# Kernel tuning notes

Measured on AMD Instinct MI355X. Metric: run time of the kernel, lower is better.

The kernel has to match this reference:

```python
import jax, jax.numpy as jnp
import numpy as np

B, T, E = 2, 4096, 256
H = 4
HD = E // H
W = 65  # local_size, odd window


def setup_inputs() -> dict:
    key = jax.random.key(0)
    ks = jax.random.split(key, 5)
    s = 1.0 / np.sqrt(E)
    return {
        "x": jax.random.normal(ks[0], (B, T, E), dtype=jnp.float32),
        "Wqkv": jax.random.normal(ks[1], (3 * E, E), dtype=jnp.float32) * s,
        "bqkv": jax.random.normal(ks[2], (3 * E,), dtype=jnp.float32) * s,
        "Wout": jax.random.normal(ks[3], (E, E), dtype=jnp.float32) * s,
        "bout": jax.random.normal(ks[4], (E,), dtype=jnp.float32) * s,
    }


def _to_heads(t):
    # (B, T, E) -> (B*H, T, HD), head index = b*H + h (matches torch view/transpose)
    return t.reshape(B, T, H, HD).transpose(0, 2, 1, 3).reshape(B * H, T, HD)


def reference(x, Wqkv, bqkv, Wout, bout):
    scaling = float(HD) ** (-0.5)
    qkv = x @ Wqkv.T + bqkv                       # (B, T, 3E)
    q, k, v = jnp.split(qkv, 3, axis=-1)
    q = _to_heads(q * scaling)                    # (BH, T, HD)
    k = _to_heads(k)
    v = _to_heads(v)
    pad = (W - 1) // 2
    kp = jnp.pad(k, ((0, 0), (pad, pad), (0, 0)))  # (BH, T+W-1, HD)
    vp = jnp.pad(v, ((0, 0), (pad, pad), (0, 0)))
    idx = jnp.arange(T)[:, None] + jnp.arange(W)[None, :]  # (T, W)
    kw = kp[:, idx, :]                            # (BH, T, W, HD) overlapping windows
    vw = vp[:, idx, :]
    scores = jnp.einsum('btd,btwd->btw', q, kw)   # (BH, T, W)
    attn = jax.nn.softmax(scores, axis=-1)
    out = jnp.einsum('btw,btwd->btd', attn, vw)   # (BH, T, HD)
    out = out.reshape(B, H, T, HD).transpose(0, 2, 1, 3).reshape(B, T, E)
    return out @ Wout.T + bout
```

## Files before the change

### kernel.cpp

```cpp
#include <hip/hip_runtime.h>
#include <hip/hip_bf16.h>
#include <math.h>

#define T_   4096
#define E_   256
#define H_   4
#define HD_  64

typedef __attribute__((ext_vector_type(8))) short short8;
typedef __attribute__((ext_vector_type(4))) float f32x4;
typedef unsigned int u32;
typedef unsigned short ushort_t;

typedef const __attribute__((address_space(1))) u32* gas_ptr;
typedef __attribute__((address_space(3))) u32* las_ptr;

__device__ __forceinline__ void gld_lds16(const void* g, void* l) {
    __builtin_amdgcn_global_load_lds((gas_ptr)g, (las_ptr)l, 16, 0, 0);
}

__device__ __forceinline__ float bf_lo(u32 w) { return __uint_as_float(w << 16); }
__device__ __forceinline__ float bf_hi(u32 w) { return __uint_as_float(w & 0xffff0000u); }
__device__ __forceinline__ ushort_t f2bf(float f) {
    __hip_bfloat16 h = __float2bfloat16(f);
    return *reinterpret_cast<ushort_t*>(&h);
}

__global__ __launch_bounds__(256) void cvt_kernel(
    const float* __restrict__ x, const float* __restrict__ wq,
    const float* __restrict__ wo,
    ushort_t* __restrict__ xb, ushort_t* __restrict__ wqb, ushort_t* __restrict__ wob)
{
    int idx = blockIdx.x * 256 + threadIdx.x;
    const float* src; ushort_t* dst; int off;
    if (idx < 262144)       { src = x;  dst = xb;  off = idx * 8; }
    else if (idx < 286720)  { src = wq; dst = wqb; off = (idx - 262144) * 8; }
    else                    { src = wo; dst = wob; off = (idx - 286720) * 8; }
    float4 a = *(const float4*)(src + off);
    float4 b = *(const float4*)(src + off + 4);
    short8 p;
    p[0] = (short)f2bf(a.x); p[1] = (short)f2bf(a.y);
    p[2] = (short)f2bf(a.z); p[3] = (short)f2bf(a.w);
    p[4] = (short)f2bf(b.x); p[5] = (short)f2bf(b.y);
    p[6] = (short)f2bf(b.z); p[7] = (short)f2bf(b.w);
    *(short8*)(dst + off) = p;
}

template<int MODE>
__global__ __launch_bounds__(256) void gemm_kernel(
    const char* __restrict__ A, const char* __restrict__ Bw,
    const float* __restrict__ bias,
    ushort_t* __restrict__ o0, ushort_t* __restrict__ o1, ushort_t* __restrict__ o2,
    float* __restrict__ of)
{
    __shared__ __align__(16) char As[2][16384];
    __shared__ __align__(16) char Bs[2][8192];
    const int tid  = threadIdx.x;
    const int lane = tid & 63;
    const int wid  = tid >> 6;
    const int m0   = blockIdx.y * 128;
    const int bx   = blockIdx.x;
    const int n0   = bx * 64;

    f32x4 acc[2][4];
    #pragma unroll
    for (int i = 0; i < 2; ++i)
        #pragma unroll
        for (int j = 0; j < 4; ++j)
            acc[i][j] = (f32x4){0.f, 0.f, 0.f, 0.f};

    auto stage = [&](int buf, int ks) {
        const int kb = ks * 128;
        #pragma unroll
        for (int i = 0; i < 4; ++i) {
            int u   = wid * 4 + i;
            int o   = u * 1024 + lane * 16;
            int row = o >> 7;
            int cb  = o & 127;
            int sc  = cb ^ ((row & 7) << 4);
            gld_lds16(A + (size_t)(m0 + row) * 512 + kb + sc, &As[buf][u * 1024]);
        }
        #pragma unroll
        for (int i = 0; i < 2; ++i) {
            int u   = wid * 2 + i;
            int o   = u * 1024 + lane * 16;
            int row = o >> 7;
            int cb  = o & 127;
            int sc  = cb ^ ((row & 7) << 4);
            gld_lds16(Bw + (size_t)(n0 + row) * 512 + kb + sc, &Bs[buf][u * 1024]);
        }
    };

    auto compute = [&](int buf) {
        #pragma unroll
        for (int k2 = 0; k2 < 2; ++k2) {
            short8 af[2], bfr[4];
            #pragma unroll
            for (int mf = 0; mf < 2; ++mf) {
                int row = wid * 32 + mf * 16 + (lane & 15);
                int off = (k2 * 64 + (lane >> 4) * 16) ^ ((row & 7) << 4);
                af[mf] = *(const short8*)(&As[buf][row * 128 + off]);
            }
            #pragma unroll
            for (int nf = 0; nf < 4; ++nf) {
                int row = nf * 16 + (lane & 15);
                int off = (k2 * 64 + (lane >> 4) * 16) ^ ((row & 7) << 4);
                bfr[nf] = *(const short8*)(&Bs[buf][row * 128 + off]);
            }
            #pragma unroll
            for (int mf = 0; mf < 2; ++mf)
                #pragma unroll
                for (int nf = 0; nf < 4; ++nf)
                    acc[mf][nf] = __builtin_amdgcn_mfma_f32_16x16x32_bf16(
                        af[mf], bfr[nf], acc[mf][nf], 0, 0, 0);
        }
    };

    stage(0, 0);
    __syncthreads();
    #pragma unroll
    for (int t = 0; t < 4; ++t) {
        if (t < 3) stage((t + 1) & 1, t + 1);
        compute(t & 1);
        __syncthreads();
    }

    if (MODE == 0) {
        const int which = bx >> 2;
        const int h     = bx & 3;
        ushort_t* dst = (which == 0) ? o0 : (which == 1) ? o1 : o2;
        const float scale = (which == 0) ? 0.125f : 1.0f;
        #pragma unroll
        for (int nf = 0; nf < 4; ++nf) {
            int d = nf * 16 + (lane & 15);
            float bv = bias[n0 + d];
            #pragma unroll
            for (int mf = 0; mf < 2; ++mf)
                #pragma unroll
                for (int r = 0; r < 4; ++r) {
                    int m  = m0 + wid * 32 + mf * 16 + (lane >> 4) * 4 + r;
                    int bb = m >> 12;
                    int t  = m & (T_ - 1);
                    float v = (acc[mf][nf][r] + bv) * scale;
                    dst[((size_t)(bb * H_ + h) * T_ + t) * HD_ + d] = f2bf(v);
                }
        }
    } else {
        #pragma unroll
        for (int nf = 0; nf < 4; ++nf) {
            int n = n0 + nf * 16 + (lane & 15);
            float bv = bias[n];
            #pragma unroll
            for (int mf = 0; mf < 2; ++mf)
                #pragma unroll
                for (int r = 0; r < 4; ++r) {
                    int m = m0 + wid * 32 + mf * 16 + (lane >> 4) * 4 + r;
                    of[(size_t)m * E_ + n] = acc[mf][nf][r] + bv;
                }
        }
    }
}

__global__ __launch_bounds__(256) void attn_kernel(
    const ushort_t* __restrict__ q, const ushort_t* __restrict__ k,
    const ushort_t* __restrict__ v, ushort_t* __restrict__ ao)
{
    __shared__ __align__(16) char smem[20480 + 25600];
    char* Ks = smem;
    char* Pb = smem;
    char* Vt = smem + 20480;

    const int tid = threadIdx.x;
    const int bh  = blockIdx.y;
    const int t0  = blockIdx.x * 64;
    const int kbase = t0 - 32;
    const char* kb = (const char*)(k + (size_t)bh * T_ * HD_);
    const char* vb = (const char*)(v + (size_t)bh * T_ * HD_);
    const char* qb = (const char*)(q + (size_t)bh * T_ * HD_);

    int4 kreg[5], vreg[5];
    #pragma unroll
    for (int l = 0; l < 5; ++l) {
        int u = tid + l * 256;
        int row = u >> 3;
        int g = kbase + row;
        bool ok = (unsigned)g < (unsigned)T_;
        kreg[l] = ok ? *(const int4*)(kb + (size_t)g * 128 + (u & 7) * 16)
                     : make_int4(0, 0, 0, 0);
        vreg[l] = ok ? *(const int4*)(vb + (size_t)g * 128 + (u & 7) * 16)
                     : make_int4(0, 0, 0, 0);
    }
    #pragma unroll
    for (int l = 0; l < 5; ++l) {
        int u = tid + l * 256;
        int row = u >> 3;
        int cb = (u & 7) * 16;
        *(int4*)(Ks + row * 128 + (cb ^ ((row & 7) << 4))) = kreg[l];
        const u32* wv = (const u32*)&vreg[l];
        #pragma unroll
        for (int j = 0; j < 8; ++j) {
            int d = (u & 7) * 8 + j;
            ushort_t h = (j & 1) ? (ushort_t)(wv[j >> 1] >> 16)
                                 : (ushort_t)(wv[j >> 1] & 0xffffu);
            *(ushort_t*)(Vt + d * 400 + ((row * 2) ^ (((d >> 3) & 7) << 4))) = h;
        }
    }
    __syncthreads();

    const int wv_ = tid >> 6;
    const int ln  = tid & 15;
    const int lg  = (tid & 63) >> 4;

    short8 qf[2];
    #pragma unroll
    for (int k2 = 0; k2 < 2; ++k2)
        qf[k2] = *(const short8*)(qb + (size_t)(t0 + wv_ * 16 + ln) * 128
                                  + k2 * 64 + lg * 16);

    f32x4 sa[6];
    #pragma unroll
    for (int nf = 0; nf < 6; ++nf) sa[nf] = (f32x4){0.f, 0.f, 0.f, 0.f};
    #pragma unroll
    for (int k2 = 0; k2 < 2; ++k2) {
        #pragma unroll
        for (int nf = 0; nf < 6; ++nf) {
            int row = wv_ * 16 + nf * 16 + ln;
            short8 kf = *(const short8*)(Ks + row * 128 +
                          ((k2 * 64 + lg * 16) ^ ((row & 7) << 4)));
            sa[nf] = __builtin_amdgcn_mfma_f32_16x16x32_bf16(qf[k2], kf, sa[nf], 0, 0, 0);
        }
    }

    const int nm0 = ln - 4 * lg;
    #pragma unroll
    for (int nf = 0; nf < 6; ++nf)
        #pragma unroll
        for (int r = 0; r < 4; ++r) {
            int diff = nm0 + 16 * nf - r;
            if (diff < 0 || diff > 64) sa[nf][r] = -1e30f;
        }
    float inv_[4];
    #pragma unroll
    for (int r = 0; r < 4; ++r) {
        float mx = sa[0][r];
        #pragma unroll
        for (int nf = 1; nf < 6; ++nf) mx = fmaxf(mx, sa[nf][r]);
        mx = fmaxf(mx, __shfl_xor(mx, 1));
        mx = fmaxf(mx, __shfl_xor(mx, 2));
        mx = fmaxf(mx, __shfl_xor(mx, 4));
        mx = fmaxf(mx, __shfl_xor(mx, 8));
        float s = 0.f;
        #pragma unroll
        for (int nf = 0; nf < 6; ++nf) {
            float e = __expf(sa[nf][r] - mx);
            sa[nf][r] = e;
            s += e;
        }
        s += __shfl_xor(s, 1);
        s += __shfl_xor(s, 2);
        s += __shfl_xor(s, 4);
        s += __shfl_xor(s, 8);
        inv_[r] = 1.f / s;
    }

    __syncthreads();
    char* Pw = Pb + wv_ * 3328;
    #pragma unroll
    for (int nf = 0; nf < 6; ++nf)
        #pragma unroll
        for (int r = 0; r < 4; ++r)
            *(ushort_t*)(Pw + (4 * lg + r) * 208 + (16 * nf + ln) * 2)
                = f2bf(sa[nf][r]);

    f32x4 oa[4];
    #pragma unroll
    for (int nf = 0; nf < 4; ++nf) oa[nf] = (f32x4){0.f, 0.f, 0.f, 0.f};
    #pragma unroll
    for (int ks = 0; ks < 3; ++ks) {
        short8 pa = *(const short8*)(Pw + ln * 208 + ks * 64 + lg * 16);
        #pragma unroll
        for (int nf = 0; nf < 4; ++nf) {
            int d = nf * 16 + ln;
            short8 vbf = *(const short8*)(Vt + d * 400 +
                           ((32 * wv_ + 64 * ks + 16 * lg) ^ (((d >> 3) & 7) << 4)));
            oa[nf] = __builtin_amdgcn_mfma_f32_16x16x32_bf16(pa, vbf, oa[nf], 0, 0, 0);
        }
    }

    const int bb = bh >> 2, hh = bh & 3;
    #pragma unroll
    for (int nf = 0; nf < 4; ++nf)
        #pragma unroll
        for (int r = 0; r < 4; ++r) {
            int t = t0 + wv_ * 16 + 4 * lg + r;
            int d = nf * 16 + ln;
            ao[((size_t)bb * T_ + t) * E_ + hh * HD_ + d] = f2bf(oa[nf][r] * inv_[r]);
        }
}

extern "C" void kernel_launch(void* const* d_in, const int* in_sizes, int n_in,
                              void* d_out, int out_size, void* d_ws, size_t ws_size,
                              hipStream_t stream) {
    const float* x    = (const float*)d_in[0];
    const float* Wqkv = (const float*)d_in[1];
    const float* bqkv = (const float*)d_in[2];
    const float* Wout = (const float*)d_in[3];
    const float* bout = (const float*)d_in[4];
    float* out = (float*)d_out;

    char* ws = (char*)d_ws;
    ushort_t* xb  = (ushort_t*)(ws);
    ushort_t* wqb = (ushort_t*)(ws + 4194304);
    ushort_t* wob = (ushort_t*)(ws + 4587520);
    ushort_t* qb  = (ushort_t*)(ws + 4718592);
    ushort_t* kbp = (ushort_t*)(ws + 8912896);
    ushort_t* vbp = (ushort_t*)(ws + 13107200);
    ushort_t* aob = (ushort_t*)(ws + 17301504);

    cvt_kernel<<<1152, 256, 0, stream>>>(x, Wqkv, Wout, xb, wqb, wob);
    gemm_kernel<0><<<dim3(12, 64), 256, 0, stream>>>(
        (const char*)xb, (const char*)wqb, bqkv, qb, kbp, vbp, nullptr);
    attn_kernel<<<dim3(64, 8), 256, 0, stream>>>(qb, kbp, vbp, aob);
    gemm_kernel<1><<<dim3(4, 64), 256, 0, stream>>>(
        (const char*)aob, (const char*)wob, bout, nullptr, nullptr, nullptr, out);
}
```

Before: 34.46 us.

## Shrink GEMM M-tile to 64 and load full K slab at once

The GEMM kernel drops from 128-row tiles with a double-buffered K loop to 64-row tiles that load the whole K=256 slab of A and B into 64 KB of LDS in one shot, then run 8 MFMA steps. The grid doubles in the M dimension, so there are twice as many blocks to fill the CUs, and the per-step pipeline syncs go away. In exchange there is no overlap between loads and compute inside a block, B is reloaded twice as often, and the larger LDS footprint lowers occupancy per CU.

```diff
diff --git a/kernel.cpp b/kernel.cpp
--- a/kernel.cpp
+++ b/kernel.cpp
@@ -19,8 +19,6 @@
     __builtin_amdgcn_global_load_lds((gas_ptr)g, (las_ptr)l, 16, 0, 0);
 }
 
-__device__ __forceinline__ float bf_lo(u32 w) { return __uint_as_float(w << 16); }
-__device__ __forceinline__ float bf_hi(u32 w) { return __uint_as_float(w & 0xffff0000u); }
 __device__ __forceinline__ ushort_t f2bf(float f) {
     __hip_bfloat16 h = __float2bfloat16(f);
     return *reinterpret_cast<ushort_t*>(&h);
@@ -53,76 +51,53 @@
     ushort_t* __restrict__ o0, ushort_t* __restrict__ o1, ushort_t* __restrict__ o2,
     float* __restrict__ of)
 {
-    __shared__ __align__(16) char As[2][16384];
-    __shared__ __align__(16) char Bs[2][8192];
+    __shared__ __align__(16) char As[32768];
+    __shared__ __align__(16) char Bs[32768];
     const int tid  = threadIdx.x;
     const int lane = tid & 63;
     const int wid  = tid >> 6;
-    const int m0   = blockIdx.y * 128;
+    const int m0   = blockIdx.y * 64;
     const int bx   = blockIdx.x;
     const int n0   = bx * 64;
 
-    f32x4 acc[2][4];
-    #pragma unroll
-    for (int i = 0; i < 2; ++i)
-        #pragma unroll
-        for (int j = 0; j < 4; ++j)
-            acc[i][j] = (f32x4){0.f, 0.f, 0.f, 0.f};
-
-    auto stage = [&](int buf, int ks) {
-        const int kb = ks * 128;
-        #pragma unroll
-        for (int i = 0; i < 4; ++i) {
-            int u   = wid * 4 + i;
-            int o   = u * 1024 + lane * 16;
-            int row = o >> 7;
-            int cb  = o & 127;
-            int sc  = cb ^ ((row & 7) << 4);
-            gld_lds16(A + (size_t)(m0 + row) * 512 + kb + sc, &As[buf][u * 1024]);
-        }
-        #pragma unroll
-        for (int i = 0; i < 2; ++i) {
-            int u   = wid * 2 + i;
-            int o   = u * 1024 + lane * 16;
-            int row = o >> 7;
-            int cb  = o & 127;
-            int sc  = cb ^ ((row & 7) << 4);
-            gld_lds16(Bw + (size_t)(n0 + row) * 512 + kb + sc, &Bs[buf][u * 1024]);
-        }
-    };
-
-    auto compute = [&](int buf) {
-        #pragma unroll
-        for (int k2 = 0; k2 < 2; ++k2) {
-            short8 af[2], bfr[4];
-            #pragma unroll
-            for (int mf = 0; mf < 2; ++mf) {
-                int row = wid * 32 + mf * 16 + (lane & 15);
-                int off = (k2 * 64 + (lane >> 4) * 16) ^ ((row & 7) << 4);
-                af[mf] = *(const short8*)(&As[buf][row * 128 + off]);
-            }
-            #pragma unroll
-            for (int nf = 0; nf < 4; ++nf) {
-                int row = nf * 16 + (lane & 15);
-                int off = (k2 * 64 + (lane >> 4) * 16) ^ ((row & 7) << 4);
-                bfr[nf] = *(const short8*)(&Bs[buf][row * 128 + off]);
-            }
-            #pragma unroll
-            for (int mf = 0; mf < 2; ++mf)
-                #pragma unroll
-                for (int nf = 0; nf < 4; ++nf)
-                    acc[mf][nf] = __builtin_amdgcn_mfma_f32_16x16x32_bf16(
-                        af[mf], bfr[nf], acc[mf][nf], 0, 0, 0);
-        }
-    };
-
-    stage(0, 0);
+    #pragma unroll
+    for (int i = 0; i < 8; ++i) {
+        int u   = wid * 8 + i;
+        int o   = u * 1024 + lane * 16;
+        int row = o >> 9;
+        int cb  = o & 511;
+        int sc  = cb ^ ((row & 7) << 4);
+        gld_lds16(A + (size_t)(m0 + row) * 512 + sc, &As[u * 1024]);
+    }
+    #pragma unroll
+    for (int i = 0; i < 8; ++i) {
+        int u   = wid * 8 + i;
+        int o   = u * 1024 + lane * 16;
+        int row = o >> 9;
+        int cb  = o & 511;
+        int sc  = cb ^ ((row & 7) << 4);
+        gld_lds16(Bw + (size_t)(n0 + row) * 512 + sc, &Bs[u * 1024]);
+    }
     __syncthreads();
-    #pragma unroll
-    for (int t = 0; t < 4; ++t) {
-        if (t < 3) stage((t + 1) & 1, t + 1);
-        compute(t & 1);
-        __syncthreads();
+
+    const int ln = lane & 15;
+    const int lg = lane >> 4;
+    const int arow = wid * 16 + ln;
+
+    f32x4 acc[4];
+    #pragma unroll
+    for (int j = 0; j < 4; ++j) acc[j] = (f32x4){0.f, 0.f, 0.f, 0.f};
+
+    #pragma unroll
+    for (int ks = 0; ks < 8; ++ks) {
+        const int koff = ks * 64 + lg * 16;
+        short8 af = *(const short8*)(&As[arow * 512 + (koff ^ ((arow & 7) << 4))]);
+        #pragma unroll
+        for (int nf = 0; nf < 4; ++nf) {
+            int brow = nf * 16 + ln;
+            short8 bf = *(const short8*)(&Bs[brow * 512 + (koff ^ ((brow & 7) << 4))]);
+            acc[nf] = __builtin_amdgcn_mfma_f32_16x16x32_bf16(af, bf, acc[nf], 0, 0, 0);
+        }
     }
 
     if (MODE == 0) {
@@ -132,31 +107,27 @@
         const float scale = (which == 0) ? 0.125f : 1.0f;
         #pragma unroll
         for (int nf = 0; nf < 4; ++nf) {
-            int d = nf * 16 + (lane & 15);
+            int d = nf * 16 + ln;
             float bv = bias[n0 + d];
             #pragma unroll
-            for (int mf = 0; mf < 2; ++mf)
-                #pragma unroll
-                for (int r = 0; r < 4; ++r) {
-                    int m  = m0 + wid * 32 + mf * 16 + (lane >> 4) * 4 + r;
-                    int bb = m >> 12;
-                    int t  = m & (T_ - 1);
-                    float v = (acc[mf][nf][r] + bv) * scale;
-                    dst[((size_t)(bb * H_ + h) * T_ + t) * HD_ + d] = f2bf(v);
-                }
+            for (int r = 0; r < 4; ++r) {
+                int m  = m0 + wid * 16 + lg * 4 + r;
+                int bb = m >> 12;
+                int t  = m & (T_ - 1);
+                float v = (acc[nf][r] + bv) * scale;
+                dst[((size_t)(bb * H_ + h) * T_ + t) * HD_ + d] = f2bf(v);
+            }
         }
     } else {
         #pragma unroll
         for (int nf = 0; nf < 4; ++nf) {
-            int n = n0 + nf * 16 + (lane & 15);
+            int n = n0 + nf * 16 + ln;
             float bv = bias[n];
             #pragma unroll
-            for (int mf = 0; mf < 2; ++mf)
-                #pragma unroll
-                for (int r = 0; r < 4; ++r) {
-                    int m = m0 + wid * 32 + mf * 16 + (lane >> 4) * 4 + r;
-                    of[(size_t)m * E_ + n] = acc[mf][nf][r] + bv;
-                }
+            for (int r = 0; r < 4; ++r) {
+                int m = m0 + wid * 16 + lg * 4 + r;
+                of[(size_t)m * E_ + n] = acc[nf][r] + bv;
+            }
         }
     }
 }
@@ -318,9 +289,9 @@
     ushort_t* aob = (ushort_t*)(ws + 17301504);
 
     cvt_kernel<<<1152, 256, 0, stream>>>(x, Wqkv, Wout, xb, wqb, wob);
-    gemm_kernel<0><<<dim3(12, 64), 256, 0, stream>>>(
+    gemm_kernel<0><<<dim3(12, 128), 256, 0, stream>>>(
         (const char*)xb, (const char*)wqb, bqkv, qb, kbp, vbp, nullptr);
     attn_kernel<<<dim3(64, 8), 256, 0, stream>>>(qb, kbp, vbp, aob);
-    gemm_kernel<1><<<dim3(4, 64), 256, 0, stream>>>(
+    gemm_kernel<1><<<dim3(4, 128), 256, 0, stream>>>(
         (const char*)aob, (const char*)wob, bout, nullptr, nullptr, nullptr, out);
 }
```

After: 36.59 us. 1.06x slower.

## Fuse fp32-to-bf16 conversion into GEMM loads and drop separate convert kernel

Applied to the files above, without the earlier changes.

Removes the standalone conversion kernel. The GEMMs now read fp32 activations and weights directly into registers, pack them to bf16 and write swizzled LDS tiles, with the register loads for the next k-step overlapping the current MFMA compute. The output projection also uses a smaller M tile (64 rows, twice the blocks) so more blocks are in flight. The QKV GEMM re-reads and re-converts fp32 x from global memory once per N-block (12 times), and each block moves twice the bytes of the bf16 path, trading that extra traffic for one fewer launch and no intermediate round trip.

```diff
diff --git a/kernel.cpp b/kernel.cpp
--- a/kernel.cpp
+++ b/kernel.cpp
@@ -19,96 +19,114 @@
     __builtin_amdgcn_global_load_lds((gas_ptr)g, (las_ptr)l, 16, 0, 0);
 }
 
-__device__ __forceinline__ float bf_lo(u32 w) { return __uint_as_float(w << 16); }
-__device__ __forceinline__ float bf_hi(u32 w) { return __uint_as_float(w & 0xffff0000u); }
 __device__ __forceinline__ ushort_t f2bf(float f) {
     __hip_bfloat16 h = __float2bfloat16(f);
     return *reinterpret_cast<ushort_t*>(&h);
 }
 
-__global__ __launch_bounds__(256) void cvt_kernel(
-    const float* __restrict__ x, const float* __restrict__ wq,
-    const float* __restrict__ wo,
-    ushort_t* __restrict__ xb, ushort_t* __restrict__ wqb, ushort_t* __restrict__ wob)
-{
-    int idx = blockIdx.x * 256 + threadIdx.x;
-    const float* src; ushort_t* dst; int off;
-    if (idx < 262144)       { src = x;  dst = xb;  off = idx * 8; }
-    else if (idx < 286720)  { src = wq; dst = wqb; off = (idx - 262144) * 8; }
-    else                    { src = wo; dst = wob; off = (idx - 286720) * 8; }
-    float4 a = *(const float4*)(src + off);
-    float4 b = *(const float4*)(src + off + 4);
+__device__ __forceinline__ short8 pack8(float4 a, float4 b) {
     short8 p;
     p[0] = (short)f2bf(a.x); p[1] = (short)f2bf(a.y);
     p[2] = (short)f2bf(a.z); p[3] = (short)f2bf(a.w);
     p[4] = (short)f2bf(b.x); p[5] = (short)f2bf(b.y);
     p[6] = (short)f2bf(b.z); p[7] = (short)f2bf(b.w);
-    *(short8*)(dst + off) = p;
-}
-
-template<int MODE>
+    return p;
+}
+
+template<int MODE, int MF>
 __global__ __launch_bounds__(256) void gemm_kernel(
-    const char* __restrict__ A, const char* __restrict__ Bw,
+    const void* __restrict__ Ain, const float* __restrict__ Bw,
     const float* __restrict__ bias,
     ushort_t* __restrict__ o0, ushort_t* __restrict__ o1, ushort_t* __restrict__ o2,
     float* __restrict__ of)
 {
-    __shared__ __align__(16) char As[2][16384];
+    constexpr bool CVTA = (MODE == 0);
+    __shared__ __align__(16) char As[2][MF * 8192];
     __shared__ __align__(16) char Bs[2][8192];
     const int tid  = threadIdx.x;
     const int lane = tid & 63;
     const int wid  = tid >> 6;
-    const int m0   = blockIdx.y * 128;
+    const int m0   = blockIdx.y * (MF * 64);
     const int bx   = blockIdx.x;
     const int n0   = bx * 64;
-
-    f32x4 acc[2][4];
-    #pragma unroll
-    for (int i = 0; i < 2; ++i)
-        #pragma unroll
-        for (int j = 0; j < 4; ++j)
-            acc[i][j] = (f32x4){0.f, 0.f, 0.f, 0.f};
-
-    auto stage = [&](int buf, int ks) {
-        const int kb = ks * 128;
-        #pragma unroll
-        for (int i = 0; i < 4; ++i) {
-            int u   = wid * 4 + i;
+    const int ln   = lane & 15;
+    const int lg   = lane >> 4;
+
+    float4 ar[MF][4];
+    float4 br[4];
+
+    auto load_regs = [&](int ks) {
+        const int k0 = ks * 64;
+        if constexpr (CVTA) {
+            #pragma unroll
+            for (int c = 0; c < MF; ++c) {
+                int u = c * 256 + tid;
+                int row = u >> 2, kq = u & 3;
+                const float4* s = (const float4*)((const float*)Ain
+                                   + (size_t)(m0 + row) * 256 + k0 + kq * 16);
+                ar[c][0] = s[0]; ar[c][1] = s[1]; ar[c][2] = s[2]; ar[c][3] = s[3];
+            }
+        }
+        int row = tid >> 2, kq = tid & 3;
+        const float4* s = (const float4*)(Bw + (size_t)(n0 + row) * 256 + k0 + kq * 16);
+        br[0] = s[0]; br[1] = s[1]; br[2] = s[2]; br[3] = s[3];
+    };
+
+    auto stage_A_lds = [&](int buf, int ks) {
+        #pragma unroll
+        for (int i = 0; i < MF * 2; ++i) {
+            int u   = wid * (MF * 2) + i;
             int o   = u * 1024 + lane * 16;
             int row = o >> 7;
             int cb  = o & 127;
             int sc  = cb ^ ((row & 7) << 4);
-            gld_lds16(A + (size_t)(m0 + row) * 512 + kb + sc, &As[buf][u * 1024]);
-        }
-        #pragma unroll
-        for (int i = 0; i < 2; ++i) {
-            int u   = wid * 2 + i;
-            int o   = u * 1024 + lane * 16;
-            int row = o >> 7;
-            int cb  = o & 127;
-            int sc  = cb ^ ((row & 7) << 4);
-            gld_lds16(Bw + (size_t)(n0 + row) * 512 + kb + sc, &Bs[buf][u * 1024]);
+            gld_lds16((const char*)Ain + (size_t)(m0 + row) * 512 + ks * 128 + sc,
+                      &As[buf][u * 1024]);
         }
     };
 
+    auto write_lds = [&](int buf) {
+        if constexpr (CVTA) {
+            #pragma unroll
+            for (int c = 0; c < MF; ++c) {
+                int u = c * 256 + tid;
+                int row = u >> 2, kq = u & 3;
+                int bb = kq * 32, sw = (row & 7) << 4;
+                *(short8*)(&As[buf][row * 128 + (bb ^ sw)])        = pack8(ar[c][0], ar[c][1]);
+                *(short8*)(&As[buf][row * 128 + ((bb + 16) ^ sw)]) = pack8(ar[c][2], ar[c][3]);
+            }
+        }
+        int row = tid >> 2, kq = tid & 3;
+        int bb = kq * 32, sw = (row & 7) << 4;
+        *(short8*)(&Bs[buf][row * 128 + (bb ^ sw)])        = pack8(br[0], br[1]);
+        *(short8*)(&Bs[buf][row * 128 + ((bb + 16) ^ sw)]) = pack8(br[2], br[3]);
+    };
+
+    f32x4 acc[MF][4];
+    #pragma unroll
+    for (int i = 0; i < MF; ++i)
+        #pragma unroll
+        for (int j = 0; j < 4; ++j)
+            acc[i][j] = (f32x4){0.f, 0.f, 0.f, 0.f};
+
     auto compute = [&](int buf) {
         #pragma unroll
         for (int k2 = 0; k2 < 2; ++k2) {
-            short8 af[2], bfr[4];
-            #pragma unroll
-            for (int mf = 0; mf < 2; ++mf) {
-                int row = wid * 32 + mf * 16 + (lane & 15);
-                int off = (k2 * 64 + (lane >> 4) * 16) ^ ((row & 7) << 4);
+            short8 af[MF], bfr[4];
+            #pragma unroll
+            for (int mf = 0; mf < MF; ++mf) {
+                int row = wid * (16 * MF) + mf * 16 + ln;
+                int off = (k2 * 64 + lg * 16) ^ ((row & 7) << 4);
                 af[mf] = *(const short8*)(&As[buf][row * 128 + off]);
             }
             #pragma unroll
             for (int nf = 0; nf < 4; ++nf) {
-                int row = nf * 16 + (lane & 15);
-                int off = (k2 * 64 + (lane >> 4) * 16) ^ ((row & 7) << 4);
+                int row = nf * 16 + ln;
+                int off = (k2 * 64 + lg * 16) ^ ((row & 7) << 4);
                 bfr[nf] = *(const short8*)(&Bs[buf][row * 128 + off]);
             }
             #pragma unroll
-            for (int mf = 0; mf < 2; ++mf)
+            for (int mf = 0; mf < MF; ++mf)
                 #pragma unroll
                 for (int nf = 0; nf < 4; ++nf)
                     acc[mf][nf] = __builtin_amdgcn_mfma_f32_16x16x32_bf16(
@@ -116,12 +134,18 @@
         }
     };
 
-    stage(0, 0);
+    load_regs(0);
+    if constexpr (!CVTA) stage_A_lds(0, 0);
+    write_lds(0);
     __syncthreads();
     #pragma unroll
     for (int t = 0; t < 4; ++t) {
-        if (t < 3) stage((t + 1) & 1, t + 1);
+        if (t < 3) {
+            load_regs(t + 1);
+            if constexpr (!CVTA) stage_A_lds((t + 1) & 1, t + 1);
+        }
         compute(t & 1);
+        if (t < 3) write_lds((t + 1) & 1);
         __syncthreads();
     }
 
@@ -132,13 +156,13 @@
         const float scale = (which == 0) ? 0.125f : 1.0f;
         #pragma unroll
         for (int nf = 0; nf < 4; ++nf) {
-            int d = nf * 16 + (lane & 15);
+            int d = nf * 16 + ln;
             float bv = bias[n0 + d];
             #pragma unroll
-            for (int mf = 0; mf < 2; ++mf)
+            for (int mf = 0; mf < MF; ++mf)
                 #pragma unroll
                 for (int r = 0; r < 4; ++r) {
-                    int m  = m0 + wid * 32 + mf * 16 + (lane >> 4) * 4 + r;
+                    int m  = m0 + wid * (16 * MF) + mf * 16 + lg * 4 + r;
                     int bb = m >> 12;
                     int t  = m & (T_ - 1);
                     float v = (acc[mf][nf][r] + bv) * scale;
@@ -148,13 +172,13 @@
     } else {
         #pragma unroll
         for (int nf = 0; nf < 4; ++nf) {
-            int n = n0 + nf * 16 + (lane & 15);
+            int n = n0 + nf * 16 + ln;
             float bv = bias[n];
             #pragma unroll
-            for (int mf = 0; mf < 2; ++mf)
+            for (int mf = 0; mf < MF; ++mf)
                 #pragma unroll
                 for (int r = 0; r < 4; ++r) {
-                    int m = m0 + wid * 32 + mf * 16 + (lane >> 4) * 4 + r;
+                    int m = m0 + wid * (16 * MF) + mf * 16 + lg * 4 + r;
                     of[(size_t)m * E_ + n] = acc[mf][nf][r] + bv;
                 }
         }
@@ -309,18 +333,14 @@
     float* out = (float*)d_out;
 
     char* ws = (char*)d_ws;
-    ushort_t* xb  = (ushort_t*)(ws);
-    ushort_t* wqb = (ushort_t*)(ws + 4194304);
-    ushort_t* wob = (ushort_t*)(ws + 4587520);
-    ushort_t* qb  = (ushort_t*)(ws + 4718592);
-    ushort_t* kbp = (ushort_t*)(ws + 8912896);
-    ushort_t* vbp = (ushort_t*)(ws + 13107200);
-    ushort_t* aob = (ushort_t*)(ws + 17301504);
-
-    cvt_kernel<<<1152, 256, 0, stream>>>(x, Wqkv, Wout, xb, wqb, wob);
-    gemm_kernel<0><<<dim3(12, 64), 256, 0, stream>>>(
-        (const char*)xb, (const char*)wqb, bqkv, qb, kbp, vbp, nullptr);
+    ushort_t* qb  = (ushort_t*)(ws);
+    ushort_t* kbp = (ushort_t*)(ws + 4194304);
+    ushort_t* vbp = (ushort_t*)(ws + 8388608);
+    ushort_t* aob = (ushort_t*)(ws + 12582912);
+
+    gemm_kernel<0, 2><<<dim3(12, 64), 256, 0, stream>>>(
+        (const void*)x, Wqkv, bqkv, qb, kbp, vbp, nullptr);
     attn_kernel<<<dim3(64, 8), 256, 0, stream>>>(qb, kbp, vbp, aob);
-    gemm_kernel<1><<<dim3(4, 64), 256, 0, stream>>>(
-        (const char*)aob, (const char*)wob, bout, nullptr, nullptr, nullptr, out);
-}
+    gemm_kernel<1, 1><<<dim3(4, 128), 256, 0, stream>>>(
+        (const void*)aob, Wout, bout, nullptr, nullptr, nullptr, out);
+}
```

Result: slower. 36.94 us (+7.2%).

## Fuse local attention with output projection into one kernel

Applied to the files above, without the earlier changes.

Merges the attention kernel and the output-projection GEMM into a single kernel. Each block now covers 32 timesteps across all 4 heads of a batch, with one wave per head, so the full 256-wide attention output row stays in LDS and is multiplied by Wout directly. This removes the bf16 attention-output round trip through global memory and one kernel launch. In exchange it uses larger LDS per block (about 118KB), fewer blocks (256), re-loads K/V windows with 3x overlap per 32 rows, and reads Wout fragments straight from global memory without staging.

```diff
diff --git a/kernel.cpp b/kernel.cpp
--- a/kernel.cpp
+++ b/kernel.cpp
@@ -12,6 +12,8 @@
 typedef unsigned int u32;
 typedef unsigned short ushort_t;
 
+#define VT_PITCH 272
+
 typedef const __attribute__((address_space(1))) u32* gas_ptr;
 typedef __attribute__((address_space(3))) u32* las_ptr;
 
@@ -19,8 +21,6 @@
     __builtin_amdgcn_global_load_lds((gas_ptr)g, (las_ptr)l, 16, 0, 0);
 }
 
-__device__ __forceinline__ float bf_lo(u32 w) { return __uint_as_float(w << 16); }
-__device__ __forceinline__ float bf_hi(u32 w) { return __uint_as_float(w & 0xffff0000u); }
 __device__ __forceinline__ ushort_t f2bf(float f) {
     __hip_bfloat16 h = __float2bfloat16(f);
     return *reinterpret_cast<ushort_t*>(&h);
@@ -46,12 +46,10 @@
     *(short8*)(dst + off) = p;
 }
 
-template<int MODE>
-__global__ __launch_bounds__(256) void gemm_kernel(
+__global__ __launch_bounds__(256) void qkv_kernel(
     const char* __restrict__ A, const char* __restrict__ Bw,
     const float* __restrict__ bias,
-    ushort_t* __restrict__ o0, ushort_t* __restrict__ o1, ushort_t* __restrict__ o2,
-    float* __restrict__ of)
+    ushort_t* __restrict__ o0, ushort_t* __restrict__ o1, ushort_t* __restrict__ o2)
 {
     __shared__ __align__(16) char As[2][16384];
     __shared__ __align__(16) char Bs[2][8192];
@@ -61,6 +59,8 @@
     const int m0   = blockIdx.y * 128;
     const int bx   = blockIdx.x;
     const int n0   = bx * 64;
+    const int ln   = lane & 15;
+    const int lg   = lane >> 4;
 
     f32x4 acc[2][4];
     #pragma unroll
@@ -97,14 +97,14 @@
             short8 af[2], bfr[4];
             #pragma unroll
             for (int mf = 0; mf < 2; ++mf) {
-                int row = wid * 32 + mf * 16 + (lane & 15);
-                int off = (k2 * 64 + (lane >> 4) * 16) ^ ((row & 7) << 4);
+                int row = wid * 32 + mf * 16 + ln;
+                int off = (k2 * 64 + lg * 16) ^ ((row & 7) << 4);
                 af[mf] = *(const short8*)(&As[buf][row * 128 + off]);
             }
             #pragma unroll
             for (int nf = 0; nf < 4; ++nf) {
-                int row = nf * 16 + (lane & 15);
-                int off = (k2 * 64 + (lane >> 4) * 16) ^ ((row & 7) << 4);
+                int row = nf * 16 + ln;
+                int off = (k2 * 64 + lg * 16) ^ ((row & 7) << 4);
                 bfr[nf] = *(const short8*)(&Bs[buf][row * 128 + off]);
             }
             #pragma unroll
@@ -125,177 +125,214 @@
         __syncthreads();
     }
 
-    if (MODE == 0) {
-        const int which = bx >> 2;
-        const int h     = bx & 3;
-        ushort_t* dst = (which == 0) ? o0 : (which == 1) ? o1 : o2;
-        const float scale = (which == 0) ? 0.125f : 1.0f;
-        #pragma unroll
-        for (int nf = 0; nf < 4; ++nf) {
-            int d = nf * 16 + (lane & 15);
-            float bv = bias[n0 + d];
-            #pragma unroll
-            for (int mf = 0; mf < 2; ++mf)
-                #pragma unroll
-                for (int r = 0; r < 4; ++r) {
-                    int m  = m0 + wid * 32 + mf * 16 + (lane >> 4) * 4 + r;
-                    int bb = m >> 12;
-                    int t  = m & (T_ - 1);
-                    float v = (acc[mf][nf][r] + bv) * scale;
-                    dst[((size_t)(bb * H_ + h) * T_ + t) * HD_ + d] = f2bf(v);
-                }
-        }
-    } else {
-        #pragma unroll
-        for (int nf = 0; nf < 4; ++nf) {
-            int n = n0 + nf * 16 + (lane & 15);
-            float bv = bias[n];
-            #pragma unroll
-            for (int mf = 0; mf < 2; ++mf)
-                #pragma unroll
-                for (int r = 0; r < 4; ++r) {
-                    int m = m0 + wid * 32 + mf * 16 + (lane >> 4) * 4 + r;
-                    of[(size_t)m * E_ + n] = acc[mf][nf][r] + bv;
-                }
-        }
-    }
-}
-
-__global__ __launch_bounds__(256) void attn_kernel(
+    const int which = bx >> 2;
+    const int h     = bx & 3;
+    ushort_t* dst = (which == 0) ? o0 : (which == 1) ? o1 : o2;
+    const float scale = (which == 0) ? 0.125f : 1.0f;
+    #pragma unroll
+    for (int nf = 0; nf < 4; ++nf) {
+        int d = nf * 16 + ln;
+        float bv = bias[n0 + d];
+        #pragma unroll
+        for (int mf = 0; mf < 2; ++mf)
+            #pragma unroll
+            for (int r = 0; r < 4; ++r) {
+                int m  = m0 + wid * 32 + mf * 16 + lg * 4 + r;
+                int bb = m >> 12;
+                int t  = m & (T_ - 1);
+                float v = (acc[mf][nf][r] + bv) * scale;
+                dst[((size_t)(bb * H_ + h) * T_ + t) * HD_ + d] = f2bf(v);
+            }
+    }
+}
+
+__global__ __launch_bounds__(256) void attnproj_kernel(
     const ushort_t* __restrict__ q, const ushort_t* __restrict__ k,
-    const ushort_t* __restrict__ v, ushort_t* __restrict__ ao)
+    const ushort_t* __restrict__ v, const ushort_t* __restrict__ wob,
+    const float* __restrict__ bout, float* __restrict__ out)
 {
-    __shared__ __align__(16) char smem[20480 + 25600];
+    __shared__ __align__(16) char smem[49152 + 4 * 64 * VT_PITCH];
     char* Ks = smem;
-    char* Pb = smem;
-    char* Vt = smem + 20480;
+    char* Vt = smem + 49152;
 
     const int tid = threadIdx.x;
-    const int bh  = blockIdx.y;
-    const int t0  = blockIdx.x * 64;
+    const int b   = blockIdx.y;
+    const int t0  = blockIdx.x * 32;
     const int kbase = t0 - 32;
-    const char* kb = (const char*)(k + (size_t)bh * T_ * HD_);
-    const char* vb = (const char*)(v + (size_t)bh * T_ * HD_);
-    const char* qb = (const char*)(q + (size_t)bh * T_ * HD_);
-
-    int4 kreg[5], vreg[5];
-    #pragma unroll
-    for (int l = 0; l < 5; ++l) {
-        int u = tid + l * 256;
-        int row = u >> 3;
-        int g = kbase + row;
-        bool ok = (unsigned)g < (unsigned)T_;
-        kreg[l] = ok ? *(const int4*)(kb + (size_t)g * 128 + (u & 7) * 16)
-                     : make_int4(0, 0, 0, 0);
-        vreg[l] = ok ? *(const int4*)(vb + (size_t)g * 128 + (u & 7) * 16)
-                     : make_int4(0, 0, 0, 0);
-    }
-    #pragma unroll
-    for (int l = 0; l < 5; ++l) {
-        int u = tid + l * 256;
-        int row = u >> 3;
-        int cb = (u & 7) * 16;
-        *(int4*)(Ks + row * 128 + (cb ^ ((row & 7) << 4))) = kreg[l];
-        const u32* wv = (const u32*)&vreg[l];
-        #pragma unroll
-        for (int j = 0; j < 8; ++j) {
-            int d = (u & 7) * 8 + j;
-            ushort_t h = (j & 1) ? (ushort_t)(wv[j >> 1] >> 16)
-                                 : (ushort_t)(wv[j >> 1] & 0xffffu);
-            *(ushort_t*)(Vt + d * 400 + ((row * 2) ^ (((d >> 3) & 7) << 4))) = h;
-        }
-    }
-    __syncthreads();
-
     const int wv_ = tid >> 6;
     const int ln  = tid & 15;
     const int lg  = (tid & 63) >> 4;
 
-    short8 qf[2];
+    int4 kreg[12], vreg[12];
+    #pragma unroll
+    for (int l = 0; l < 12; ++l) {
+        int u = tid + l * 256;
+        int ru = u >> 3;
+        int h = ru / 96;
+        int krow = ru - h * 96;
+        int c = u & 7;
+        int g = kbase + krow;
+        bool ok = (unsigned)g < (unsigned)T_;
+        size_t base = ((size_t)(b * 4 + h) * T_ + (ok ? g : 0)) * 128 + c * 16;
+        kreg[l] = ok ? *(const int4*)((const char*)k + base) : make_int4(0, 0, 0, 0);
+        vreg[l] = ok ? *(const int4*)((const char*)v + base) : make_int4(0, 0, 0, 0);
+    }
+    short8 qf[2][2];
+    #pragma unroll
+    for (int mf = 0; mf < 2; ++mf)
+        #pragma unroll
+        for (int k2 = 0; k2 < 2; ++k2)
+            qf[mf][k2] = *(const short8*)((const char*)q +
+                ((size_t)(b * 4 + wv_) * T_ + t0 + mf * 16 + ln) * 128
+                + k2 * 64 + lg * 16);
+
+    #pragma unroll
+    for (int l = 0; l < 12; ++l) {
+        int u = tid + l * 256;
+        int ru = u >> 3;
+        int h = ru / 96;
+        int krow = ru - h * 96;
+        int c = u & 7;
+        *(int4*)(Ks + (h * 96 + krow) * 128 + ((c * 16) ^ ((krow & 7) << 4))) = kreg[l];
+        const u32* wvp = (const u32*)&vreg[l];
+        #pragma unroll
+        for (int j = 0; j < 8; ++j) {
+            int d = c * 8 + j;
+            ushort_t hv = (j & 1) ? (ushort_t)(wvp[j >> 1] >> 16)
+                                  : (ushort_t)(wvp[j >> 1] & 0xffffu);
+            *(ushort_t*)(Vt + (size_t)(h * 64 + d) * VT_PITCH +
+                         ((krow * 2) ^ (((d >> 3) & 7) << 4))) = hv;
+        }
+    }
+    __syncthreads();
+
+    f32x4 sa[2][6];
+    #pragma unroll
+    for (int mf = 0; mf < 2; ++mf)
+        #pragma unroll
+        for (int nf = 0; nf < 6; ++nf) sa[mf][nf] = (f32x4){0.f, 0.f, 0.f, 0.f};
     #pragma unroll
     for (int k2 = 0; k2 < 2; ++k2)
-        qf[k2] = *(const short8*)(qb + (size_t)(t0 + wv_ * 16 + ln) * 128
-                                  + k2 * 64 + lg * 16);
-
-    f32x4 sa[6];
-    #pragma unroll
-    for (int nf = 0; nf < 6; ++nf) sa[nf] = (f32x4){0.f, 0.f, 0.f, 0.f};
-    #pragma unroll
-    for (int k2 = 0; k2 < 2; ++k2) {
         #pragma unroll
         for (int nf = 0; nf < 6; ++nf) {
-            int row = wv_ * 16 + nf * 16 + ln;
-            short8 kf = *(const short8*)(Ks + row * 128 +
-                          ((k2 * 64 + lg * 16) ^ ((row & 7) << 4)));
-            sa[nf] = __builtin_amdgcn_mfma_f32_16x16x32_bf16(qf[k2], kf, sa[nf], 0, 0, 0);
-        }
-    }
-
-    const int nm0 = ln - 4 * lg;
-    #pragma unroll
-    for (int nf = 0; nf < 6; ++nf)
+            int krow = nf * 16 + ln;
+            short8 kf = *(const short8*)(Ks + (wv_ * 96 + krow) * 128 +
+                            ((k2 * 64 + lg * 16) ^ ((krow & 7) << 4)));
+            sa[0][nf] = __builtin_amdgcn_mfma_f32_16x16x32_bf16(qf[0][k2], kf, sa[0][nf], 0, 0, 0);
+            sa[1][nf] = __builtin_amdgcn_mfma_f32_16x16x32_bf16(qf[1][k2], kf, sa[1][nf], 0, 0, 0);
+        }
+
+    float inv_[2][4];
+    #pragma unroll
+    for (int mf = 0; mf < 2; ++mf)
         #pragma unroll
         for (int r = 0; r < 4; ++r) {
-            int diff = nm0 + 16 * nf - r;
-            if (diff < 0 || diff > 64) sa[nf][r] = -1e30f;
-        }
-    float inv_[4];
-    #pragma unroll
-    for (int r = 0; r < 4; ++r) {
-        float mx = sa[0][r];
-        #pragma unroll
-        for (int nf = 1; nf < 6; ++nf) mx = fmaxf(mx, sa[nf][r]);
-        mx = fmaxf(mx, __shfl_xor(mx, 1));
-        mx = fmaxf(mx, __shfl_xor(mx, 2));
-        mx = fmaxf(mx, __shfl_xor(mx, 4));
-        mx = fmaxf(mx, __shfl_xor(mx, 8));
-        float s = 0.f;
-        #pragma unroll
-        for (int nf = 0; nf < 6; ++nf) {
-            float e = __expf(sa[nf][r] - mx);
-            sa[nf][r] = e;
-            s += e;
-        }
-        s += __shfl_xor(s, 1);
-        s += __shfl_xor(s, 2);
-        s += __shfl_xor(s, 4);
-        s += __shfl_xor(s, 8);
-        inv_[r] = 1.f / s;
-    }
-
-    __syncthreads();
-    char* Pw = Pb + wv_ * 3328;
-    #pragma unroll
-    for (int nf = 0; nf < 6; ++nf)
-        #pragma unroll
-        for (int r = 0; r < 4; ++r)
-            *(ushort_t*)(Pw + (4 * lg + r) * 208 + (16 * nf + ln) * 2)
-                = f2bf(sa[nf][r]);
-
-    f32x4 oa[4];
-    #pragma unroll
-    for (int nf = 0; nf < 4; ++nf) oa[nf] = (f32x4){0.f, 0.f, 0.f, 0.f};
+            int m = mf * 16 + 4 * lg + r;
+            #pragma unroll
+            for (int nf = 0; nf < 6; ++nf) {
+                int diff = nf * 16 + ln - m;
+                if (diff < 0 || diff > 64) sa[mf][nf][r] = -1e30f;
+            }
+            float mx = sa[mf][0][r];
+            #pragma unroll
+            for (int nf = 1; nf < 6; ++nf) mx = fmaxf(mx, sa[mf][nf][r]);
+            mx = fmaxf(mx, __shfl_xor(mx, 1));
+            mx = fmaxf(mx, __shfl_xor(mx, 2));
+            mx = fmaxf(mx, __shfl_xor(mx, 4));
+            mx = fmaxf(mx, __shfl_xor(mx, 8));
+            float su = 0.f;
+            #pragma unroll
+            for (int nf = 0; nf < 6; ++nf) {
+                float e = __expf(sa[mf][nf][r] - mx);
+                sa[mf][nf][r] = e;
+                su += e;
+            }
+            su += __shfl_xor(su, 1);
+            su += __shfl_xor(su, 2);
+            su += __shfl_xor(su, 4);
+            su += __shfl_xor(su, 8);
+            inv_[mf][r] = 1.f / su;
+        }
+
+    char* Pw = Ks + wv_ * 12288;
+    #pragma unroll
+    for (int mf = 0; mf < 2; ++mf)
+        #pragma unroll
+        for (int nf = 0; nf < 6; ++nf)
+            #pragma unroll
+            for (int r = 0; r < 4; ++r)
+                *(ushort_t*)(Pw + (mf * 16 + 4 * lg + r) * 208 + (nf * 16 + ln) * 2)
+                    = f2bf(sa[mf][nf][r]);
+
+    f32x4 oa[2][4];
+    #pragma unroll
+    for (int mf = 0; mf < 2; ++mf)
+        #pragma unroll
+        for (int nf = 0; nf < 4; ++nf) oa[mf][nf] = (f32x4){0.f, 0.f, 0.f, 0.f};
     #pragma unroll
     for (int ks = 0; ks < 3; ++ks) {
-        short8 pa = *(const short8*)(Pw + ln * 208 + ks * 64 + lg * 16);
+        short8 pa0 = *(const short8*)(Pw + ln * 208 + ks * 64 + lg * 16);
+        short8 pa1 = *(const short8*)(Pw + (16 + ln) * 208 + ks * 64 + lg * 16);
         #pragma unroll
         for (int nf = 0; nf < 4; ++nf) {
             int d = nf * 16 + ln;
-            short8 vbf = *(const short8*)(Vt + d * 400 +
-                           ((32 * wv_ + 64 * ks + 16 * lg) ^ (((d >> 3) & 7) << 4)));
-            oa[nf] = __builtin_amdgcn_mfma_f32_16x16x32_bf16(pa, vbf, oa[nf], 0, 0, 0);
-        }
-    }
-
-    const int bb = bh >> 2, hh = bh & 3;
-    #pragma unroll
-    for (int nf = 0; nf < 4; ++nf)
-        #pragma unroll
-        for (int r = 0; r < 4; ++r) {
-            int t = t0 + wv_ * 16 + 4 * lg + r;
-            int d = nf * 16 + ln;
-            ao[((size_t)bb * T_ + t) * E_ + hh * HD_ + d] = f2bf(oa[nf][r] * inv_[r]);
-        }
+            short8 vb = *(const short8*)(Vt + (size_t)(wv_ * 64 + d) * VT_PITCH +
+                           ((ks * 64 + lg * 16) ^ (((d >> 3) & 7) << 4)));
+            oa[0][nf] = __builtin_amdgcn_mfma_f32_16x16x32_bf16(pa0, vb, oa[0][nf], 0, 0, 0);
+            oa[1][nf] = __builtin_amdgcn_mfma_f32_16x16x32_bf16(pa1, vb, oa[1][nf], 0, 0, 0);
+        }
+    }
+
+    __syncthreads();
+    char* OL = Vt;
+    #pragma unroll
+    for (int mf = 0; mf < 2; ++mf)
+        #pragma unroll
+        for (int nf = 0; nf < 4; ++nf)
+            #pragma unroll
+            for (int r = 0; r < 4; ++r) {
+                int row = mf * 16 + 4 * lg + r;
+                int col = wv_ * 64 + nf * 16 + ln;
+                *(ushort_t*)(OL + row * 512 + ((col * 2) ^ ((row & 7) << 4)))
+                    = f2bf(oa[mf][nf][r] * inv_[mf][r]);
+            }
+    __syncthreads();
+
+    f32x4 pacc[2][4];
+    #pragma unroll
+    for (int mf = 0; mf < 2; ++mf)
+        #pragma unroll
+        for (int nf = 0; nf < 4; ++nf) pacc[mf][nf] = (f32x4){0.f, 0.f, 0.f, 0.f};
+    #pragma unroll
+    for (int ks = 0; ks < 8; ++ks) {
+        short8 paf[2];
+        #pragma unroll
+        for (int mf = 0; mf < 2; ++mf) {
+            int row = mf * 16 + ln;
+            paf[mf] = *(const short8*)(OL + row * 512 +
+                          ((ks * 64 + lg * 16) ^ ((row & 7) << 4)));
+        }
+        #pragma unroll
+        for (int nf = 0; nf < 4; ++nf) {
+            short8 bf = *(const short8*)(wob + ((size_t)(wv_ * 64 + nf * 16 + ln)) * 256
+                                         + ks * 32 + lg * 8);
+            pacc[0][nf] = __builtin_amdgcn_mfma_f32_16x16x32_bf16(paf[0], bf, pacc[0][nf], 0, 0, 0);
+            pacc[1][nf] = __builtin_amdgcn_mfma_f32_16x16x32_bf16(paf[1], bf, pacc[1][nf], 0, 0, 0);
+        }
+    }
+
+    #pragma unroll
+    for (int nf = 0; nf < 4; ++nf) {
+        int eo = wv_ * 64 + nf * 16 + ln;
+        float bv = bout[eo];
+        #pragma unroll
+        for (int mf = 0; mf < 2; ++mf)
+            #pragma unroll
+            for (int r = 0; r < 4; ++r) {
+                int t = t0 + mf * 16 + 4 * lg + r;
+                out[((size_t)b * T_ + t) * E_ + eo] = pacc[mf][nf][r] + bv;
+            }
+    }
 }
 
 extern "C" void kernel_launch(void* const* d_in, const int* in_sizes, int n_in,
@@ -315,12 +352,9 @@
     ushort_t* qb  = (ushort_t*)(ws + 4718592);
     ushort_t* kbp = (ushort_t*)(ws + 8912896);
     ushort_t* vbp = (ushort_t*)(ws + 13107200);
-    ushort_t* aob = (ushort_t*)(ws + 17301504);
 
     cvt_kernel<<<1152, 256, 0, stream>>>(x, Wqkv, Wout, xb, wqb, wob);
-    gemm_kernel<0><<<dim3(12, 64), 256, 0, stream>>>(
-        (const char*)xb, (const char*)wqb, bqkv, qb, kbp, vbp, nullptr);
-    attn_kernel<<<dim3(64, 8), 256, 0, stream>>>(qb, kbp, vbp, aob);
-    gemm_kernel<1><<<dim3(4, 64), 256, 0, stream>>>(
-        (const char*)aob, (const char*)wob, bout, nullptr, nullptr, nullptr, out);
-}
+    qkv_kernel<<<dim3(12, 64), 256, 0, stream>>>(
+        (const char*)xb, (const char*)wqb, bqkv, qb, kbp, vbp);
+    attnproj_kernel<<<dim3(128, 2), 256, 0, stream>>>(qb, kbp, vbp, wob, bout, out);
+}
```

Measured after the change: 37.50 us. 8.8% more time.
